# Kernel tuning notes

Hardware: AMD Instinct MI355X
Metric: run time of the kernel (lower is better)

Reference implementation:

```python
import jax, jax.numpy as jnp
import numpy as np

B, T, F = 4096, 60, 64
H = 128          # num_hidden[0] == num_hidden[1]
FC1_IN, FC1_OUT = T * H, 512   # 7680 -> 512
LEN_OUT = 60


def setup_inputs() -> dict:
    key = jax.random.key(0)
    ks = jax.random.split(key, 14)
    s1 = 1.0 / np.sqrt(H)
    def u(k, shape, s):
        return jax.random.uniform(k, shape, jnp.float32, -s, s)
    return {
        "X_cont": jax.random.normal(ks[0], (B, T, F), jnp.float32),
        # LSTM layer 1 (PyTorch gate order i,f,g,o)
        "W_ih1": u(ks[1], (4 * H, F), s1),
        "W_hh1": u(ks[2], (4 * H, H), s1),
        "b_ih1": u(ks[3], (4 * H,), s1),
        "b_hh1": u(ks[4], (4 * H,), s1),
        # LSTM layer 2
        "W_ih2": u(ks[5], (4 * H, H), s1),
        "W_hh2": u(ks[6], (4 * H, H), s1),
        "b_ih2": u(ks[7], (4 * H,), s1),
        "b_hh2": u(ks[8], (4 * H,), s1),
        # FC head
        "W_fc1": u(ks[9], (FC1_OUT, FC1_IN), 1.0 / np.sqrt(FC1_IN)),
        "b_fc1": u(ks[10], (FC1_OUT,), 1.0 / np.sqrt(FC1_IN)),
        "W_fc2": u(ks[11], (LEN_OUT, FC1_OUT), 1.0 / np.sqrt(FC1_OUT)),
        "b_fc2": u(ks[12], (LEN_OUT,), 1.0 / np.sqrt(FC1_OUT)),
    }


def _lstm_layer(x, W_ih, W_hh, b_ih, b_hh):
    # x: [B,T,Fin]; zero initial (h,c); returns full hidden sequence [B,T,H]
    b, h = x.shape[0], W_hh.shape[1]
    # precompute input contribution for all timesteps (one big GEMM)
    xg = jnp.einsum('btf,gf->btg', x, W_ih) + b_ih + b_hh  # [B,T,4H]

    def step(carry, xt):
        hp, cp = carry
        g = xt + hp @ W_hh.T                                # [B,4H]
        i, f, gg, o = jnp.split(g, 4, axis=-1)
        i = jax.nn.sigmoid(i)
        f = jax.nn.sigmoid(f)
        gg = jnp.tanh(gg)
        o = jax.nn.sigmoid(o)
        c = f * cp + i * gg
        hn = o * jnp.tanh(c)
        return (hn, c), hn

    h0 = jnp.zeros((b, h), x.dtype)
    _, hs = jax.lax.scan(step, (h0, h0), jnp.swapaxes(xg, 0, 1))  # [T,B,H]
    return jnp.swapaxes(hs, 0, 1)


def reference(X_cont, W_ih1, W_hh1, b_ih1, b_hh1,
              W_ih2, W_hh2, b_ih2, b_hh2,
              W_fc1, b_fc1, W_fc2, b_fc2):
    b = X_cont.shape[0]
    h1 = _lstm_layer(X_cont, W_ih1, W_hh1, b_ih1, b_hh1)   # [B,T,H]
    h2 = _lstm_layer(h1, W_ih2, W_hh2, b_ih2, b_hh2)       # [B,T,H]
    flat = h2.reshape(b, -1)                               # [B, T*H] = [B,7680]
    fc1 = flat @ W_fc1.T + b_fc1                           # [B,512]
    fc2 = fc1 @ W_fc2.T + b_fc2                            # [B,length_out]
    return fc2.reshape(b, LEN_OUT, 1)
```

## Files before the change

kernel.cpp:

```cpp
#include <hip/hip_runtime.h>
#include <hip/hip_fp16.h>
#include <cstdint>

typedef _Float16 h16;
typedef _Float16 half8 __attribute__((ext_vector_type(8)));
typedef float floatx4 __attribute__((ext_vector_type(4)));

#define T_SZ 60
#define H_SZ 128
#define NB_FC1 7680

#define LOG2E  1.44269504088896340736f
#define LOG2E2 2.88539008177792681472f

__device__ __forceinline__ float sigm(float x) {
    float e = __builtin_amdgcn_exp2f(x * -LOG2E);
    return __builtin_amdgcn_rcpf(1.0f + e);
}
__device__ __forceinline__ float tanh_fast(float x) {
    float e = __builtin_amdgcn_exp2f(x * LOG2E2);
    return 1.0f - 2.0f * __builtin_amdgcn_rcpf(e + 1.0f);
}

template<int INDIM, bool IN_F32>
__global__ __launch_bounds__(512, 1)
void lstm_layer(const void* __restrict__ in_v,
                const float* __restrict__ W_ih,
                const float* __restrict__ W_hh,
                const float* __restrict__ b_ih,
                const float* __restrict__ b_hh,
                h16* __restrict__ h_out)
{
    constexpr int KT_IN = INDIM / 32;
    __shared__ __align__(16) h16 hist[16][16][H_SZ];

    const int tid  = threadIdx.x;
    const int w    = tid >> 6;
    const int lane = tid & 63;
    const int lrow = lane & 15;
    const int lgrp = lane >> 4;
    const size_t base_row = (size_t)blockIdx.x * 16;

    half8 wf_in[4][KT_IN];
    half8 wf_hh[4][4];
    float bias[4];

    #pragma unroll
    for (int q = 0; q < 4; ++q) {
        const int n = (w + 8 * q) * 16 + lrow;
        bias[q] = b_ih[n] + b_hh[n];
        #pragma unroll
        for (int kt = 0; kt < KT_IN; ++kt) {
            const float* p = W_ih + (size_t)n * INDIM + kt * 32 + lgrp * 8;
            half8 v;
            #pragma unroll
            for (int j = 0; j < 8; ++j) v[j] = (h16)p[j];
            wf_in[q][kt] = v;
        }
        #pragma unroll
        for (int kt = 0; kt < 4; ++kt) {
            const float* p = W_hh + (size_t)n * H_SZ + kt * 32 + lgrp * 8;
            half8 v;
            #pragma unroll
            for (int j = 0; j < 8; ++j) v[j] = (h16)p[j];
            wf_hh[q][kt] = v;
        }
    }

    const float* inF = (const float*)in_v;
    const h16*   inH = (const h16*)in_v;

    floatx4 raw[KT_IN][2];
    half8   xs[KT_IN];

    auto load_x = [&](int t) {
        #pragma unroll
        for (int kt = 0; kt < KT_IN; ++kt) {
            if constexpr (IN_F32) {
                const float* p = inF + ((base_row + lrow) * T_SZ + t) * INDIM + kt * 32 + lgrp * 8;
                raw[kt][0] = *(const floatx4*)(p);
                raw[kt][1] = *(const floatx4*)(p + 4);
            } else {
                xs[kt] = *(const half8*)(inH + ((base_row + lrow) * T_SZ + t) * INDIM + kt * 32 + lgrp * 8);
            }
        }
    };

    auto get_x = [&](half8 (&xf)[KT_IN]) {
        #pragma unroll
        for (int kt = 0; kt < KT_IN; ++kt) {
            if constexpr (IN_F32) {
                const auto p0 = __builtin_amdgcn_cvt_pkrtz(raw[kt][0][0], raw[kt][0][1]);
                const auto p1 = __builtin_amdgcn_cvt_pkrtz(raw[kt][0][2], raw[kt][0][3]);
                const auto p2 = __builtin_amdgcn_cvt_pkrtz(raw[kt][1][0], raw[kt][1][1]);
                const auto p3 = __builtin_amdgcn_cvt_pkrtz(raw[kt][1][2], raw[kt][1][3]);
                half8 v;
                v[0] = (h16)p0[0]; v[1] = (h16)p0[1]; v[2] = (h16)p1[0]; v[3] = (h16)p1[1];
                v[4] = (h16)p2[0]; v[5] = (h16)p2[1]; v[6] = (h16)p3[0]; v[7] = (h16)p3[1];
                xf[kt] = v;
            } else {
                xf[kt] = xs[kt];
            }
        }
    };

    floatx4 c4 = {0.f, 0.f, 0.f, 0.f};
    const int colW = 16 * w + lrow;

    auto flush = [&](int t) {
        half8 vals[4];
        int   time[4], row[4], cg[4];
        #pragma unroll
        for (int s = 0; s < 4; ++s) {
            const int u = tid + 512 * s;
            time[s] = t - 7 + (u >> 8);
            row[s]  = (u >> 4) & 15;
            cg[s]   = u & 15;
            vals[s] = *(const half8*)&hist[time[s] & 15][row[s]][(cg[s] * 8) ^ ((row[s] & 7) << 3)];
        }
        #pragma unroll
        for (int s = 0; s < 4; ++s)
            *(half8*)(h_out + ((base_row + row[s]) * T_SZ + time[s]) * H_SZ + cg[s] * 8) = vals[s];
    };

    floatx4 accA[4], accB[4];
    load_x(0);
    {
        half8 xf[KT_IN];
        get_x(xf);
        #pragma unroll
        for (int q = 0; q < 4; ++q) accA[q] = floatx4{bias[q], bias[q], bias[q], bias[q]};
        #pragma unroll
        for (int kt = 0; kt < KT_IN; ++kt)
            #pragma unroll
            for (int q = 0; q < 4; ++q)
                accA[q] = __builtin_amdgcn_mfma_f32_16x16x32_f16(xf[kt], wf_in[q][kt], accA[q], 0, 0, 0);
        load_x(1);
    }

    auto step = [&](int t, floatx4 (&accC)[4], floatx4 (&accN)[4]) {
        half8 hf[4];
        const bool have_h = (t > 0);
        if (have_h) {
            const h16* hb = &hist[(t - 1) & 15][0][0];
            #pragma unroll
            for (int kt = 0; kt < 4; ++kt) {
                const int col0 = kt * 32 + lgrp * 8;
                hf[kt] = *(const half8*)(hb + lrow * H_SZ + (col0 ^ ((lrow & 7) << 3)));
            }
        }

        if (t + 1 < T_SZ) {
            half8 xf[KT_IN];
            get_x(xf);
            #pragma unroll
            for (int q = 0; q < 4; ++q) accN[q] = floatx4{bias[q], bias[q], bias[q], bias[q]};
            #pragma unroll
            for (int kt = 0; kt < KT_IN; ++kt)
                #pragma unroll
                for (int q = 0; q < 4; ++q)
                    accN[q] = __builtin_amdgcn_mfma_f32_16x16x32_f16(xf[kt], wf_in[q][kt], accN[q], 0, 0, 0);
            if (t + 2 < T_SZ) load_x(t + 2);
        }

        if (have_h) {
            #pragma unroll
            for (int kt = 0; kt < 4; ++kt)
                #pragma unroll
                for (int q = 0; q < 4; ++q)
                    accC[q] = __builtin_amdgcn_mfma_f32_16x16x32_f16(hf[kt], wf_hh[q][kt], accC[q], 0, 0, 0);
        }

        h16 hcast[4];
        #pragma unroll
        for (int r = 0; r < 4; ++r) {
            const float gi = sigm(accC[0][r]);
            const float gf = sigm(accC[1][r]);
            const float gg = tanh_fast(accC[2][r]);
            const float go = sigm(accC[3][r]);
            const float cc = gf * c4[r] + gi * gg;
            c4[r] = cc;
            hcast[r] = (h16)(go * tanh_fast(cc));
        }
        h16* hb2 = &hist[t & 15][0][0];
        #pragma unroll
        for (int r = 0; r < 4; ++r) {
            const int rowW = lgrp * 4 + r;
            hb2[rowW * H_SZ + (colW ^ ((rowW & 7) << 3))] = hcast[r];
        }

        asm volatile("s_waitcnt lgkmcnt(0)" ::: "memory");
        __builtin_amdgcn_s_barrier();
        asm volatile("" ::: "memory");

        if (((t & 7) == 7) || (t == T_SZ - 1)) flush(t);
    };

    #pragma unroll 1
    for (int tt = 0; tt < T_SZ; tt += 2) {
        step(tt,     accA, accB);
        step(tt + 1, accB, accA);
    }
}

__global__ __launch_bounds__(256, 2)
void head_kernel(const float* __restrict__ W_fc1,
                 const float* __restrict__ W_fc2,
                 const float* __restrict__ b_fc1,
                 const float* __restrict__ b_fc2,
                 h16* __restrict__ Wc,
                 float* __restrict__ bc)
{
    const int tid  = threadIdx.x;
    if (blockIdx.x >= 120) {
        const int m = blockIdx.x - 120;
        const int t = tid;
        float p = W_fc2[m * 512 + t] * b_fc1[t] + W_fc2[m * 512 + 256 + t] * b_fc1[256 + t];
        #pragma unroll
        for (int off = 1; off < 64; off <<= 1) p += __shfl_xor(p, off);
        __shared__ float sred[4];
        if ((t & 63) == 0) sred[t >> 6] = p;
        __syncthreads();
        if (t == 0) bc[m] = sred[0] + sred[1] + sred[2] + sred[3] + b_fc2[m];
        return;
    }

    const int wv   = tid >> 6;
    const int lane = tid & 63;
    const int lrow = lane & 15;
    const int lgrp = lane >> 4;
    const int j0   = blockIdx.x * 64 + wv * 16;

    floatx4 acc[4];
    #pragma unroll
    for (int mt = 0; mt < 4; ++mt) acc[mt] = floatx4{0.f, 0.f, 0.f, 0.f};

    for (int kt = 0; kt < 16; ++kt) {
        const int k0 = kt * 32 + lgrp * 8;
        half8 bf;
        #pragma unroll
        for (int i = 0; i < 8; ++i)
            bf[i] = (h16)W_fc1[(size_t)(k0 + i) * NB_FC1 + j0 + lrow];
        #pragma unroll
        for (int mt = 0; mt < 4; ++mt) {
            const int m = mt * 16 + lrow;
            half8 af = {};
            if (m < 60) {
                const float* p = W_fc2 + (size_t)m * 512 + k0;
                const floatx4 f0 = *(const floatx4*)(p);
                const floatx4 f1 = *(const floatx4*)(p + 4);
                const auto p0 = __builtin_amdgcn_cvt_pkrtz(f0[0], f0[1]);
                const auto p1 = __builtin_amdgcn_cvt_pkrtz(f0[2], f0[3]);
                const auto p2 = __builtin_amdgcn_cvt_pkrtz(f1[0], f1[1]);
                const auto p3 = __builtin_amdgcn_cvt_pkrtz(f1[2], f1[3]);
                af[0] = (h16)p0[0]; af[1] = (h16)p0[1]; af[2] = (h16)p1[0]; af[3] = (h16)p1[1];
                af[4] = (h16)p2[0]; af[5] = (h16)p2[1]; af[6] = (h16)p3[0]; af[7] = (h16)p3[1];
            }
            acc[mt] = __builtin_amdgcn_mfma_f32_16x16x32_f16(af, bf, acc[mt], 0, 0, 0);
        }
    }

    #pragma unroll
    for (int mt = 0; mt < 4; ++mt)
        #pragma unroll
        for (int r = 0; r < 4; ++r) {
            const int m = mt * 16 + lgrp * 4 + r;
            if (m < 60) Wc[(size_t)m * NB_FC1 + j0 + lrow] = (h16)acc[mt][r];
        }
}

__global__ __launch_bounds__(256, 2)
void fc_kernel(const h16* __restrict__ h2,
               const h16* __restrict__ Wc,
               const float* __restrict__ bcv,
               float* __restrict__ out)
{
    __shared__ float red[4][4][16][16];
    const int tid = threadIdx.x;
    const int w = tid >> 6, lane = tid & 63, lrow = lane & 15, lgrp = lane >> 4;
    const size_t base_row = (size_t)blockIdx.x * 16;

    floatx4 acc[4];
    #pragma unroll
    for (int q = 0; q < 4; ++q) acc[q] = floatx4{0.f, 0.f, 0.f, 0.f};

    const h16* arow = h2 + (base_row + lrow) * NB_FC1;
    for (int i = 0; i < 60; ++i) {
        const int kt = w * 60 + i;
        const int k0 = kt * 32 + lgrp * 8;
        const half8 a = *(const half8*)(arow + k0);
        #pragma unroll
        for (int q = 0; q < 4; ++q) {
            const int n = q * 16 + lrow;
            half8 b = 0;
            if (n < 60) b = *(const half8*)(Wc + (size_t)n * NB_FC1 + k0);
            acc[q] = __builtin_amdgcn_mfma_f32_16x16x32_f16(a, b, acc[q], 0, 0, 0);
        }
    }
    #pragma unroll
    for (int q = 0; q < 4; ++q)
        #pragma unroll
        for (int r = 0; r < 4; ++r)
            red[w][q][lgrp * 4 + r][lrow] = acc[q][r];
    __syncthreads();

    #pragma unroll
    for (int s = 0; s < 4; ++s) {
        const int idx = tid + 256 * s;
        const int row = idx >> 6, col = idx & 63;
        if (col < 60) {
            const int q = col >> 4, cin = col & 15;
            const float v = red[0][q][row][cin] + red[1][q][row][cin]
                          + red[2][q][row][cin] + red[3][q][row][cin];
            out[(base_row + row) * 60 + col] = v + bcv[col];
        }
    }
}

extern "C" void kernel_launch(void* const* d_in, const int* in_sizes, int n_in,
                              void* d_out, int out_size, void* d_ws, size_t ws_size,
                              hipStream_t stream)
{
    const float* X      = (const float*)d_in[0];
    const float* W_ih1  = (const float*)d_in[1];
    const float* W_hh1  = (const float*)d_in[2];
    const float* b_ih1  = (const float*)d_in[3];
    const float* b_hh1  = (const float*)d_in[4];
    const float* W_ih2  = (const float*)d_in[5];
    const float* W_hh2  = (const float*)d_in[6];
    const float* b_ih2  = (const float*)d_in[7];
    const float* b_hh2  = (const float*)d_in[8];
    const float* W_fc1  = (const float*)d_in[9];
    const float* b_fc1  = (const float*)d_in[10];
    const float* W_fc2  = (const float*)d_in[11];
    const float* b_fc2  = (const float*)d_in[12];

    h16* h1 = (h16*)d_ws;
    h16* h2 = h1 + (size_t)4096 * NB_FC1;
    h16* Wc = h2 + (size_t)4096 * NB_FC1;
    float* bc = (float*)(Wc + (size_t)60 * NB_FC1);

    head_kernel<<<180, 256, 0, stream>>>(W_fc1, W_fc2, b_fc1, b_fc2, Wc, bc);
    lstm_layer<64,  true ><<<256, 512, 0, stream>>>((const void*)X,  W_ih1, W_hh1, b_ih1, b_hh1, h1);
    lstm_layer<128, false><<<256, 512, 0, stream>>>((const void*)h1, W_ih2, W_hh2, b_ih2, b_hh2, h2);
    fc_kernel<<<256, 256, 0, stream>>>(h2, Wc, bc, (float*)d_out);
}
```

Measured before the change: 236.7 us.

## Fuse both LSTM layers into one kernel with flag-based wavefront pipelining

Both LSTM layers now run in a single launch of 512 blocks. Layer-1 blocks publish per-block progress flags after each 8-step window of hidden states is flushed. Layer-2 blocks spin on those flags before loading their inputs, so the second layer can overlap with the first instead of waiting for it to finish. This relies on all 512 blocks being co-resident (launch bounds changed to 2 blocks per CU) to avoid deadlock, and it adds spin-wait and release/acquire costs.

```diff
diff --git a/kernel.cpp b/kernel.cpp
--- a/kernel.cpp
+++ b/kernel.cpp
@@ -22,24 +22,24 @@
     return 1.0f - 2.0f * __builtin_amdgcn_rcpf(e + 1.0f);
 }
 
-template<int INDIM, bool IN_F32>
-__global__ __launch_bounds__(512, 1)
-void lstm_layer(const void* __restrict__ in_v,
-                const float* __restrict__ W_ih,
-                const float* __restrict__ W_hh,
-                const float* __restrict__ b_ih,
-                const float* __restrict__ b_hh,
-                h16* __restrict__ h_out)
+#define HIST(s,r,c) hist[(((s) * 16 + (r)) * H_SZ) + (c)]
+
+template<int INDIM, bool IN_F32, bool PROD>
+__device__ __forceinline__ void lstm_body(
+    const void* __restrict__ in_v,
+    const float* __restrict__ W_ih, const float* __restrict__ W_hh,
+    const float* __restrict__ b_ih, const float* __restrict__ b_hh,
+    h16* __restrict__ h_out,
+    h16* __restrict__ hist,
+    int* __restrict__ flags, int blk)
 {
     constexpr int KT_IN = INDIM / 32;
-    __shared__ __align__(16) h16 hist[16][16][H_SZ];
-
     const int tid  = threadIdx.x;
     const int w    = tid >> 6;
     const int lane = tid & 63;
     const int lrow = lane & 15;
     const int lgrp = lane >> 4;
-    const size_t base_row = (size_t)blockIdx.x * 16;
+    const size_t base_row = (size_t)blk * 16;
 
     half8 wf_in[4][KT_IN];
     half8 wf_hh[4][4];
@@ -69,6 +69,22 @@
 
     const float* inF = (const float*)in_v;
     const h16*   inH = (const h16*)in_v;
+
+    int seen = 0;
+    auto wait_win = [&](int t) {
+        if constexpr (!PROD) {
+            const int need = (t >> 3) + 1;
+            while (seen < need) {
+                int v = 0;
+                if (lane == 0)
+                    v = __hip_atomic_load(&flags[blk], __ATOMIC_ACQUIRE,
+                                          __HIP_MEMORY_SCOPE_AGENT);
+                v = __shfl(v, 0);
+                seen = v;
+                if (seen < need) __builtin_amdgcn_s_sleep(8);
+            }
+        }
+    };
 
     floatx4 raw[KT_IN][2];
     half8   xs[KT_IN];
@@ -116,14 +132,23 @@
             time[s] = t - 7 + (u >> 8);
             row[s]  = (u >> 4) & 15;
             cg[s]   = u & 15;
-            vals[s] = *(const half8*)&hist[time[s] & 15][row[s]][(cg[s] * 8) ^ ((row[s] & 7) << 3)];
+            vals[s] = *(const half8*)&HIST(time[s] & 15, row[s], (cg[s] * 8) ^ ((row[s] & 7) << 3));
         }
         #pragma unroll
         for (int s = 0; s < 4; ++s)
             *(half8*)(h_out + ((base_row + row[s]) * T_SZ + time[s]) * H_SZ + cg[s] * 8) = vals[s];
+
+        if constexpr (PROD) {
+            asm volatile("s_waitcnt vmcnt(0)" ::: "memory");
+            __builtin_amdgcn_s_barrier();
+            if (tid == 0)
+                __hip_atomic_store(&flags[blk], (t >> 3) + 1, __ATOMIC_RELEASE,
+                                   __HIP_MEMORY_SCOPE_AGENT);
+        }
     };
 
     floatx4 accA[4], accB[4];
+    wait_win(1);
     load_x(0);
     {
         half8 xf[KT_IN];
@@ -142,7 +167,7 @@
         half8 hf[4];
         const bool have_h = (t > 0);
         if (have_h) {
-            const h16* hb = &hist[(t - 1) & 15][0][0];
+            const h16* hb = &HIST((t - 1) & 15, 0, 0);
             #pragma unroll
             for (int kt = 0; kt < 4; ++kt) {
                 const int col0 = kt * 32 + lgrp * 8;
@@ -160,7 +185,10 @@
                 #pragma unroll
                 for (int q = 0; q < 4; ++q)
                     accN[q] = __builtin_amdgcn_mfma_f32_16x16x32_f16(xf[kt], wf_in[q][kt], accN[q], 0, 0, 0);
-            if (t + 2 < T_SZ) load_x(t + 2);
+            if (t + 2 < T_SZ) {
+                wait_win(t + 2);
+                load_x(t + 2);
+            }
         }
 
         if (have_h) {
@@ -182,7 +210,7 @@
             c4[r] = cc;
             hcast[r] = (h16)(go * tanh_fast(cc));
         }
-        h16* hb2 = &hist[t & 15][0][0];
+        h16* hb2 = &HIST(t & 15, 0, 0);
         #pragma unroll
         for (int r = 0; r < 4; ++r) {
             const int rowW = lgrp * 4 + r;
@@ -200,6 +228,26 @@
     for (int tt = 0; tt < T_SZ; tt += 2) {
         step(tt,     accA, accB);
         step(tt + 1, accB, accA);
+    }
+}
+
+__global__ __launch_bounds__(512, 2)
+void lstm_both(const float* __restrict__ X,
+               const float* __restrict__ W_ih1, const float* __restrict__ W_hh1,
+               const float* __restrict__ b_ih1, const float* __restrict__ b_hh1,
+               const float* __restrict__ W_ih2, const float* __restrict__ W_hh2,
+               const float* __restrict__ b_ih2, const float* __restrict__ b_hh2,
+               h16* __restrict__ h1, h16* __restrict__ h2,
+               int* __restrict__ flags)
+{
+    __shared__ __align__(16) h16 hist[16 * 16 * H_SZ];
+
+    if (blockIdx.x < 256) {
+        lstm_body<64, true, true>((const void*)X, W_ih1, W_hh1, b_ih1, b_hh1,
+                                  h1, hist, flags, blockIdx.x);
+    } else {
+        lstm_body<128, false, false>((const void*)h1, W_ih2, W_hh2, b_ih2, b_hh2,
+                                     h2, hist, flags, blockIdx.x - 256);
     }
 }
 
@@ -209,11 +257,13 @@
                  const float* __restrict__ b_fc1,
                  const float* __restrict__ b_fc2,
                  h16* __restrict__ Wc,
-                 float* __restrict__ bc)
+                 float* __restrict__ bc,
+                 int* __restrict__ flags)
 {
     const int tid  = threadIdx.x;
     if (blockIdx.x >= 120) {
         const int m = blockIdx.x - 120;
+        if (m == 0) flags[tid] = 0;
         const int t = tid;
         float p = W_fc2[m * 512 + t] * b_fc1[t] + W_fc2[m * 512 + 256 + t] * b_fc1[256 + t];
         #pragma unroll
@@ -339,9 +389,10 @@
     h16* h2 = h1 + (size_t)4096 * NB_FC1;
     h16* Wc = h2 + (size_t)4096 * NB_FC1;
     float* bc = (float*)(Wc + (size_t)60 * NB_FC1);
-
-    head_kernel<<<180, 256, 0, stream>>>(W_fc1, W_fc2, b_fc1, b_fc2, Wc, bc);
-    lstm_layer<64,  true ><<<256, 512, 0, stream>>>((const void*)X,  W_ih1, W_hh1, b_ih1, b_hh1, h1);
-    lstm_layer<128, false><<<256, 512, 0, stream>>>((const void*)h1, W_ih2, W_hh2, b_ih2, b_hh2, h2);
+    int* flags = (int*)(bc + 64);
+
+    head_kernel<<<180, 256, 0, stream>>>(W_fc1, W_fc2, b_fc1, b_fc2, Wc, bc, flags);
+    lstm_both<<<512, 512, 0, stream>>>(X, W_ih1, W_hh1, b_ih1, b_hh1,
+                                       W_ih2, W_hh2, b_ih2, b_hh2, h1, h2, flags);
     fc_kernel<<<256, 256, 0, stream>>>(h2, Wc, bc, (float*)d_out);
 }
```

Result: slower. 293.7 us (+24.1%).
